# Kernel optimization log

Hardware: AMD Instinct MI355X
Metric: run time of the kernel (lower is better)

## Reference

```python
import jax, jax.numpy as jnp
import numpy as np
import math

D_MODEL = 1024
N_HEAD = 16
D_K = D_MODEL // N_HEAD
NEG_INF = -1e30  # fp32 mask fill value used by the torch module


def _rope(x, b_rotate=None):
    # x: [b, h, n, k], k even. Interleaved (even/odd) RoPE, matching the torch code.
    b, h, n, k = x.shape
    half = k // 2
    inv_freq = 1.0 / (10000.0 ** (jnp.arange(half, dtype=jnp.float32) / half))  # [half]
    ang = jnp.arange(n, dtype=jnp.float32)[:, None] * inv_freq[None, :]          # [n, half]
    sin = jnp.sin(ang)
    cos = jnp.cos(ang)
    x1 = x[..., 0::2]  # [b,h,n,half]
    x2 = x[..., 1::2]
    even = x1 * cos - x2 * sin
    odd = x1 * sin + x2 * cos
    out = jnp.stack([even, odd], axis=-1).reshape(b, h, n, k)  # re-interleave
    if b_rotate is not None:
        out = out * b_rotate  # barope multiplicative term
    return out


def setup_inputs() -> dict:
    key = jax.random.key(0)
    ks = jax.random.split(key, 7)
    B, S = 1, 2048
    query = jax.random.normal(ks[0], (B, S, D_MODEL), dtype=jnp.float32)
    kk = jax.random.normal(ks[1], (B, S, D_MODEL), dtype=jnp.float32)
    value = jax.random.normal(ks[2], (B, S, D_MODEL), dtype=jnp.float32)
    b_emb = jax.random.normal(ks[3], (B, S, D_MODEL), dtype=jnp.float32)
    mask = jax.random.bernoulli(ks[4], 0.9, (B, S))  # bool [B,S]
    linear_layers = 0.02 * jax.random.normal(ks[5], (3, D_MODEL, N_HEAD, D_K), dtype=jnp.float32)
    b_proj = jax.random.normal(ks[6], (D_MODEL, N_HEAD, D_K), dtype=jnp.float32)
    return {"query": query, "key": kk, "value": value, "b_emb": b_emb,
            "mask": mask, "linear_layers": linear_layers, "b_proj": b_proj}


def reference(query, key, value, b_emb, mask, linear_layers, b_proj):
    B, S, _ = query.shape
    # QKV projections: [b,n,d] x [d,h,k] -> [b,h,n,k]
    q = jnp.einsum('bnd,dhk->bhnk', query, linear_layers[0])
    k = jnp.einsum('bnd,dhk->bhnk', key, linear_layers[1])
    v = jnp.einsum('bnd,dhk->bhnk', value, linear_layers[2])
    # barope=True branch: multiplicative rotation modifier from b_emb
    b_rotate = jnp.einsum('bnd,dhk->bhnk', b_emb, b_proj)
    q = _rope(q, b_rotate)
    k = _rope(k, b_rotate)
    scores = jnp.einsum('bhqk,bhmk->bhqm', q, k) / math.sqrt(D_K)  # [b,h,s,s]
    pair_mask = (mask[:, :, None] & mask[:, None, :])[:, None]     # [b,1,s,s]
    scores = jnp.where(pair_mask, scores, NEG_INF)
    p_attn = jax.nn.softmax(scores, axis=-1)  # dropout p=0 -> identity
    x = jnp.einsum('bhqm,bhmk->bhqk', p_attn, v)
    return x.transpose(0, 2, 1, 3).reshape(B, S, N_HEAD * D_K)
```

## Files before the change

kernel.cpp:

```cpp
#include <hip/hip_runtime.h>
#include <hip/hip_bf16.h>
#include <math.h>

#define S_LEN 2048
#define NHEAD 16
#define DMODEL 1024

typedef short bf16x8 __attribute__((ext_vector_type(8)));
typedef float f32x4 __attribute__((ext_vector_type(4)));

static __device__ __forceinline__ unsigned short bfbits(float x) {
    __hip_bfloat16 h = __float2bfloat16(x);
    unsigned short u; __builtin_memcpy(&u, &h, 2); return u;
}
static __device__ __forceinline__ float bf2f(unsigned short u) {
    union { unsigned int i; float f; } v; v.i = ((unsigned int)u) << 16; return v.f;
}
static __device__ __forceinline__ void splitRN(float x, unsigned short& hi, unsigned short& lo) {
    unsigned short h = bfbits(x);
    float r = x - bf2f(h);
    hi = h; lo = bfbits(r);
}
static __device__ __forceinline__ void split4(float4 x, ushort4& h4, ushort4& l4) {
    unsigned short h0,l0,h1,l1,h2,l2,h3,l3;
    splitRN(x.x,h0,l0); splitRN(x.y,h1,l1); splitRN(x.z,h2,l2); splitRN(x.w,h3,l3);
    h4 = make_ushort4(h0,h1,h2,h3); l4 = make_ushort4(l0,l1,l2,l3);
}

__device__ __forceinline__ int mask_at(const void* mp, int enc, int s) {
    if (enc) return ((const unsigned char*)mp)[s] != 0;
    return ((const unsigned int*)mp)[s] != 0u;
}

__global__ void detect_kernel(const void* __restrict__ mask, int* __restrict__ flags) {
    if (threadIdx.x == 0 && blockIdx.x == 0) {
        const unsigned int* m = (const unsigned int*)mask;
        int bytey = 0;
        for (int i = 0; i < 8; ++i) {
            unsigned int u = m[i];
            if (u != 0u && u != 1u && u != 0x3F800000u) bytey = 1;
        }
        flags[0] = bytey;
    }
}

__global__ __launch_bounds__(256)
void presplit_w(const float* __restrict__ ll, const float* __restrict__ bproj,
                unsigned short* __restrict__ Wh, unsigned short* __restrict__ Wl) {
    __shared__ unsigned short Th[64][72], Tl[64][72];
    const int t = threadIdx.x;
    const int bid = blockIdx.x;
    const int stream = bid >> 8;
    const int rem = bid & 255;
    const int h = rem >> 4;
    const int d0 = (rem & 15) << 6;
    const float* src = (stream == 3) ? bproj : (ll + (size_t)stream * 1048576);
#pragma unroll
    for (int rep = 0; rep < 4; ++rep) {
        int fid = rep * 256 + t;
        int dl = fid >> 4, n4 = (fid & 15) * 4;
        float4 w = *(const float4*)&src[(size_t)(d0 + dl) * 1024 + h * 64 + n4];
        unsigned short hh, lo2;
#pragma unroll
        for (int m = 0; m < 4; ++m) { splitRN((&w.x)[m], hh, lo2); Th[n4+m][dl] = hh; Tl[n4+m][dl] = lo2; }
    }
    __syncthreads();
    size_t obase = (size_t)stream * 1048576;
#pragma unroll
    for (int rep = 0; rep < 2; ++rep) {
        int wid = rep * 256 + t;
        int n = wid >> 3, dl8 = (wid & 7) * 8;
        int dtile = n >> 4, cc = n & 15;
        int dglob = d0 + dl8;
        int kc = dglob >> 5;
        int qd = (dglob >> 3) & 3;
        size_t off = obase + (size_t)(h * 4 + dtile) * 16384 + (size_t)kc * 512
                   + (size_t)(qd * 16 + cc) * 8;
        *(uint4*)&Wh[off] = *(uint4*)&Th[n][dl8];
        *(uint4*)&Wl[off] = *(uint4*)&Tl[n][dl8];
    }
}

__global__ __launch_bounds__(256, 4)
void proj_fused7(const float* __restrict__ Xq, const float* __restrict__ Xk,
                 const float* __restrict__ Xv, const float* __restrict__ Xb,
                 const unsigned short* __restrict__ Wh, const unsigned short* __restrict__ Wl,
                 unsigned short* __restrict__ qhi, unsigned short* __restrict__ qlo,
                 unsigned short* __restrict__ khi, unsigned short* __restrict__ klo,
                 unsigned short* __restrict__ vhi) {
    __shared__ unsigned short smem[17920];
    unsigned short (*T0)[72] = (unsigned short(*)[72])(smem + 0);
    unsigned short (*T1)[72] = (unsigned short(*)[72])(smem + 2304);
    unsigned short (*T2)[40] = (unsigned short(*)[40])(smem + 4608);

    const int t = threadIdx.x;
    const int lin = blockIdx.x;
    const int xcd = lin & 7;
    const int inner = lin >> 3;
    const int h = inner >> 3;
    const int sg = inner & 7;
    const int s0 = (xcd * 8 + sg) * 32;
    const int lane = t & 63, dt = t >> 6, quad = lane >> 4, c = lane & 15;

    f32x4 aq[2], ak[2], av[2], ab[2];
#pragma unroll
    for (int i = 0; i < 2; ++i) {
        aq[i] = (f32x4){0.f,0.f,0.f,0.f}; ak[i] = (f32x4){0.f,0.f,0.f,0.f};
        av[i] = (f32x4){0.f,0.f,0.f,0.f}; ab[i] = (f32x4){0.f,0.f,0.f,0.f};
    }

    const int xr = t >> 3, xc = (t & 7) * 4;
    const size_t xg = (size_t)(s0 + xr) * DMODEL + xc;
    const size_t wb = (size_t)(h * 4 + dt) * 16384 + (size_t)lane * 8;

#define XARR(name, b, i) unsigned short (*name)[40] = (unsigned short(*)[40])(smem + (b) * 8960 + (i) * 1280)

    float4 pq, pk, pv, pb;
    pq = *(const float4*)&Xq[xg];
    pk = *(const float4*)&Xk[xg];
    pv = *(const float4*)&Xv[xg];
    pb = *(const float4*)&Xb[xg];
    {
        XARR(XQh,0,0); XARR(XQl,0,1); XARR(XKh,0,2); XARR(XKl,0,3);
        XARR(XVh,0,4); XARR(XBh,0,5); XARR(XBl,0,6);
        ushort4 h4, l4;
        split4(pq, h4, l4); *(ushort4*)&XQh[xr][xc] = h4; *(ushort4*)&XQl[xr][xc] = l4;
        split4(pk, h4, l4); *(ushort4*)&XKh[xr][xc] = h4; *(ushort4*)&XKl[xr][xc] = l4;
        split4(pb, h4, l4); *(ushort4*)&XBh[xr][xc] = h4; *(ushort4*)&XBl[xr][xc] = l4;
        *(ushort4*)&XVh[xr][xc] = make_ushort4(bfbits(pv.x),bfbits(pv.y),bfbits(pv.z),bfbits(pv.w));
    }
    pq = *(const float4*)&Xq[xg + 32];
    pk = *(const float4*)&Xk[xg + 32];
    pv = *(const float4*)&Xv[xg + 32];
    pb = *(const float4*)&Xb[xg + 32];
    __syncthreads();

    for (int kc = 0; kc < 32; ++kc) {
        const int cb = kc & 1, nb = cb ^ 1;
        size_t wo = wb + (size_t)kc * 512;
        bf16x8 aQh = *(const bf16x8*)&Wh[wo];
        bf16x8 aQl = *(const bf16x8*)&Wl[wo];
        bf16x8 aKh = *(const bf16x8*)&Wh[1048576 + wo];
        bf16x8 aKl = *(const bf16x8*)&Wl[1048576 + wo];
        bf16x8 aVh = *(const bf16x8*)&Wh[2097152 + wo];
        bf16x8 aVl = *(const bf16x8*)&Wl[2097152 + wo];
        bf16x8 aBh = *(const bf16x8*)&Wh[3145728 + wo];
        bf16x8 aBl = *(const bf16x8*)&Wl[3145728 + wo];

        if (kc + 1 < 32) {
            XARR(XQh,nb,0); XARR(XQl,nb,1); XARR(XKh,nb,2); XARR(XKl,nb,3);
            XARR(XVh,nb,4); XARR(XBh,nb,5); XARR(XBl,nb,6);
            ushort4 h4, l4;
            split4(pq, h4, l4); *(ushort4*)&XQh[xr][xc] = h4; *(ushort4*)&XQl[xr][xc] = l4;
            split4(pk, h4, l4); *(ushort4*)&XKh[xr][xc] = h4; *(ushort4*)&XKl[xr][xc] = l4;
            split4(pb, h4, l4); *(ushort4*)&XBh[xr][xc] = h4; *(ushort4*)&XBl[xr][xc] = l4;
            *(ushort4*)&XVh[xr][xc] = make_ushort4(bfbits(pv.x),bfbits(pv.y),bfbits(pv.z),bfbits(pv.w));
        }
        if (kc + 2 < 32) {
            size_t g = xg + (size_t)(kc + 2) * 32;
            pq = *(const float4*)&Xq[g];
            pk = *(const float4*)&Xk[g];
            pv = *(const float4*)&Xv[g];
            pb = *(const float4*)&Xb[g];
        }

        {
            XARR(XQh,cb,0); XARR(XQl,cb,1); XARR(XKh,cb,2); XARR(XKl,cb,3);
            XARR(XVh,cb,4); XARR(XBh,cb,5); XARR(XBl,cb,6);
#pragma unroll
            for (int st = 0; st < 2; ++st) {
                bf16x8 b1 = *(bf16x8*)&XQh[st*16+c][quad*8];
                bf16x8 b2 = *(bf16x8*)&XQl[st*16+c][quad*8];
                aq[st] = __builtin_amdgcn_mfma_f32_16x16x32_bf16(aQh, b1, aq[st], 0, 0, 0);
                aq[st] = __builtin_amdgcn_mfma_f32_16x16x32_bf16(aQh, b2, aq[st], 0, 0, 0);
                aq[st] = __builtin_amdgcn_mfma_f32_16x16x32_bf16(aQl, b1, aq[st], 0, 0, 0);
                b1 = *(bf16x8*)&XKh[st*16+c][quad*8];
                b2 = *(bf16x8*)&XKl[st*16+c][quad*8];
                ak[st] = __builtin_amdgcn_mfma_f32_16x16x32_bf16(aKh, b1, ak[st], 0, 0, 0);
                ak[st] = __builtin_amdgcn_mfma_f32_16x16x32_bf16(aKh, b2, ak[st], 0, 0, 0);
                ak[st] = __builtin_amdgcn_mfma_f32_16x16x32_bf16(aKl, b1, ak[st], 0, 0, 0);
                b1 = *(bf16x8*)&XVh[st*16+c][quad*8];
                av[st] = __builtin_amdgcn_mfma_f32_16x16x32_bf16(aVh, b1, av[st], 0, 0, 0);
                av[st] = __builtin_amdgcn_mfma_f32_16x16x32_bf16(aVl, b1, av[st], 0, 0, 0);
                b1 = *(bf16x8*)&XBh[st*16+c][quad*8];
                b2 = *(bf16x8*)&XBl[st*16+c][quad*8];
                ab[st] = __builtin_amdgcn_mfma_f32_16x16x32_bf16(aBh, b1, ab[st], 0, 0, 0);
                ab[st] = __builtin_amdgcn_mfma_f32_16x16x32_bf16(aBh, b2, ab[st], 0, 0, 0);
                ab[st] = __builtin_amdgcn_mfma_f32_16x16x32_bf16(aBl, b1, ab[st], 0, 0, 0);
            }
        }
        __syncthreads();
    }
#undef XARR

    float rq[2][4], rk[2][4];
    {
        int p0 = dt * 8 + 2 * quad;
        double inv0 = pow(10000.0, -(double)p0 / 32.0);
        double inv1 = pow(10000.0, -(double)(p0 + 1) / 32.0);
#pragma unroll
        for (int st = 0; st < 2; ++st) {
            int s = s0 + st * 16 + c;
            double a0 = (double)s * inv0, a1 = (double)s * inv1;
            float sn0 = (float)sin(a0), cs0 = (float)cos(a0);
            float sn1 = (float)sin(a1), cs1 = (float)cos(a1);
            rq[st][0] = (aq[st][0]*cs0 - aq[st][1]*sn0) * ab[st][0] * 0.125f;
            rq[st][1] = (aq[st][0]*sn0 + aq[st][1]*cs0) * ab[st][1] * 0.125f;
            rq[st][2] = (aq[st][2]*cs1 - aq[st][3]*sn1) * ab[st][2] * 0.125f;
            rq[st][3] = (aq[st][2]*sn1 + aq[st][3]*cs1) * ab[st][3] * 0.125f;
            rk[st][0] = (ak[st][0]*cs0 - ak[st][1]*sn0) * ab[st][0];
            rk[st][1] = (ak[st][0]*sn0 + ak[st][1]*cs0) * ab[st][1];
            rk[st][2] = (ak[st][2]*cs1 - ak[st][3]*sn1) * ab[st][2];
            rk[st][3] = (ak[st][2]*sn1 + ak[st][3]*cs1) * ab[st][3];
        }
    }
    __syncthreads();
#pragma unroll
    for (int st = 0; st < 2; ++st) {
        unsigned short h0,l0,h1,l1,h2,l2,h3,l3;
        splitRN(rq[st][0],h0,l0); splitRN(rq[st][1],h1,l1);
        splitRN(rq[st][2],h2,l2); splitRN(rq[st][3],h3,l3);
        *(ushort4*)&T0[st*16+c][dt*16+4*quad] = make_ushort4(h0,h1,h2,h3);
        *(ushort4*)&T1[st*16+c][dt*16+4*quad] = make_ushort4(l0,l1,l2,l3);
#pragma unroll
        for (int reg = 0; reg < 4; ++reg)
            T2[dt * 16 + 4 * quad + reg][st * 16 + c] = bfbits(av[st][reg]);
    }
    __syncthreads();
    {
        int row = t >> 3, d8 = (t & 7) * 8;
        size_t qb = ((size_t)(h * S_LEN + s0 + row)) * 64 + d8;
        *(uint4*)&qhi[qb] = *(uint4*)&T0[row][d8];
        *(uint4*)&qlo[qb] = *(uint4*)&T1[row][d8];
        int d = t >> 2, s8 = (t & 3) * 8;
        size_t vb = ((size_t)(h * 64 + d)) * S_LEN + s0 + s8;
        *(uint4*)&vhi[vb] = *(uint4*)&T2[d][s8];
    }
    __syncthreads();
#pragma unroll
    for (int st = 0; st < 2; ++st) {
        unsigned short h0,l0,h1,l1,h2,l2,h3,l3;
        splitRN(rk[st][0],h0,l0); splitRN(rk[st][1],h1,l1);
        splitRN(rk[st][2],h2,l2); splitRN(rk[st][3],h3,l3);
        *(ushort4*)&T0[st*16+c][dt*16+4*quad] = make_ushort4(h0,h1,h2,h3);
        *(ushort4*)&T1[st*16+c][dt*16+4*quad] = make_ushort4(l0,l1,l2,l3);
    }
    __syncthreads();
    {
        int row = t >> 3, d8 = (t & 7) * 8;
        size_t qb = ((size_t)(h * S_LEN + s0 + row)) * 64 + d8;
        *(uint4*)&khi[qb] = *(uint4*)&T0[row][d8];
        *(uint4*)&klo[qb] = *(uint4*)&T1[row][d8];
    }
}

__global__ __launch_bounds__(256)
void attn_mfma(const unsigned short* __restrict__ qh, const unsigned short* __restrict__ ql,
               const unsigned short* __restrict__ kh, const unsigned short* __restrict__ kl,
               const unsigned short* __restrict__ vh,
               const void* __restrict__ mask, float* __restrict__ out,
               const int* __restrict__ flags) {
    __shared__ unsigned short Kh[2][64][72], Kl[2][64][72];
    __shared__ unsigned short Vt[2][64][72];
    __shared__ unsigned short Sh[64][72], Sl[64][72];
    const int menc = flags[0];
    const int t = threadIdx.x;
    const int lin = blockIdx.x + (blockIdx.y << 5);
    const int h = (lin & 7) * 2 + ((lin >> 3) & 1);
    const int s0 = (lin >> 4) * 64;
    const int lane = t & 63, w = t >> 6, quad = lane >> 4, c = lane & 15;

    bf16x8 qfh[2], qfl[2];
#pragma unroll
    for (int ks = 0; ks < 2; ++ks) {
        size_t base = ((size_t)(h * S_LEN + s0 + 16 * w + c)) * 64 + ks * 32 + quad * 8;
        qfh[ks] = *(const bf16x8*)&qh[base];
        qfl[ks] = *(const bf16x8*)&ql[base];
    }
    int mq[4];
#pragma unroll
    for (int i = 0; i < 4; ++i) mq[i] = mask_at(mask, menc, s0 + 16 * w + quad * 4 + i);

    float m_i[4], l_i[4];
#pragma unroll
    for (int i = 0; i < 4; ++i) { m_i[i] = -INFINITY; l_i[i] = 0.0f; }
    f32x4 o_acc[4];
#pragma unroll
    for (int i = 0; i < 4; ++i) o_acc[i] = (f32x4){0.f,0.f,0.f,0.f};

    uint4 pre[6];
#pragma unroll
    for (int i = 0; i < 2; ++i) {
        int id = i * 256 + t, row = id >> 3, col8 = (id & 7) * 8;
        size_t kb = ((size_t)(h * S_LEN + row)) * 64 + col8;
        size_t vb = ((size_t)(h * 64 + row)) * S_LEN + col8;
        pre[0 + i] = *(const uint4*)&kh[kb];
        pre[2 + i] = *(const uint4*)&kl[kb];
        pre[4 + i] = *(const uint4*)&vh[vb];
    }
#pragma unroll
    for (int i = 0; i < 2; ++i) {
        int id = i * 256 + t, row = id >> 3, col8 = (id & 7) * 8;
        *(uint4*)&Kh[0][row][col8] = pre[0 + i];
        *(uint4*)&Kl[0][row][col8] = pre[2 + i];
        *(uint4*)&Vt[0][row][col8] = pre[4 + i];
    }
    __syncthreads();

    int cur = 0;
    for (int kt = 0; kt < 32; ++kt) {
        if (kt + 1 < 32) {
            const int kb0 = (kt + 1) * 64;
#pragma unroll
            for (int i = 0; i < 2; ++i) {
                int id = i * 256 + t, row = id >> 3, col8 = (id & 7) * 8;
                size_t kb = ((size_t)(h * S_LEN + kb0 + row)) * 64 + col8;
                size_t vb = ((size_t)(h * 64 + row)) * S_LEN + kb0 + col8;
                pre[0 + i] = *(const uint4*)&kh[kb];
                pre[2 + i] = *(const uint4*)&kl[kb];
                pre[4 + i] = *(const uint4*)&vh[vb];
            }
        }
        int mk[4];
#pragma unroll
        for (int nt = 0; nt < 4; ++nt) mk[nt] = mask_at(mask, menc, kt * 64 + 16 * nt + c);

        f32x4 sc[4];
#pragma unroll
        for (int i = 0; i < 4; ++i) sc[i] = (f32x4){0.f,0.f,0.f,0.f};
#pragma unroll
        for (int nt = 0; nt < 4; ++nt)
#pragma unroll
            for (int ks = 0; ks < 2; ++ks) {
                bf16x8 kfh = *(bf16x8*)&Kh[cur][nt * 16 + c][ks * 32 + quad * 8];
                bf16x8 kfl = *(bf16x8*)&Kl[cur][nt * 16 + c][ks * 32 + quad * 8];
                sc[nt] = __builtin_amdgcn_mfma_f32_16x16x32_bf16(qfh[ks], kfh, sc[nt], 0, 0, 0);
                sc[nt] = __builtin_amdgcn_mfma_f32_16x16x32_bf16(qfh[ks], kfl, sc[nt], 0, 0, 0);
                sc[nt] = __builtin_amdgcn_mfma_f32_16x16x32_bf16(qfl[ks], kfh, sc[nt], 0, 0, 0);
            }

        float sm[4][4];
#pragma unroll
        for (int nt = 0; nt < 4; ++nt)
#pragma unroll
            for (int reg = 0; reg < 4; ++reg)
                sm[nt][reg] = (mq[reg] && mk[nt]) ? sc[nt][reg] : -1e30f;

        float rmax[4];
#pragma unroll
        for (int reg = 0; reg < 4; ++reg)
            rmax[reg] = fmaxf(fmaxf(sm[0][reg], sm[1][reg]), fmaxf(sm[2][reg], sm[3][reg]));
#pragma unroll
        for (int off = 1; off <= 8; off <<= 1)
#pragma unroll
            for (int reg = 0; reg < 4; ++reg)
                rmax[reg] = fmaxf(rmax[reg], __shfl_xor(rmax[reg], off, 64));

        float mn[4], alpha[4];
#pragma unroll
        for (int reg = 0; reg < 4; ++reg) {
            mn[reg] = fmaxf(m_i[reg], rmax[reg]);
            alpha[reg] = __expf(m_i[reg] - mn[reg]);
            m_i[reg] = mn[reg];
        }

        float rsum[4] = {0.f, 0.f, 0.f, 0.f};
#pragma unroll
        for (int nt = 0; nt < 4; ++nt)
#pragma unroll
            for (int reg = 0; reg < 4; ++reg) {
                float e = __expf(sm[nt][reg] - mn[reg]);
                rsum[reg] += e;
                unsigned short eh, el;
                splitRN(e, eh, el);
                Sh[16 * w + quad * 4 + reg][16 * nt + c] = eh;
                Sl[16 * w + quad * 4 + reg][16 * nt + c] = el;
            }
#pragma unroll
        for (int off = 1; off <= 8; off <<= 1)
#pragma unroll
            for (int reg = 0; reg < 4; ++reg)
                rsum[reg] += __shfl_xor(rsum[reg], off, 64);
#pragma unroll
        for (int reg = 0; reg < 4; ++reg) l_i[reg] = l_i[reg] * alpha[reg] + rsum[reg];
#pragma unroll
        for (int nt = 0; nt < 4; ++nt)
#pragma unroll
            for (int reg = 0; reg < 4; ++reg) o_acc[nt][reg] *= alpha[reg];

        if (kt + 1 < 32) {
            const int nxt = cur ^ 1;
#pragma unroll
            for (int i = 0; i < 2; ++i) {
                int id = i * 256 + t, row = id >> 3, col8 = (id & 7) * 8;
                *(uint4*)&Kh[nxt][row][col8] = pre[0 + i];
                *(uint4*)&Kl[nxt][row][col8] = pre[2 + i];
                *(uint4*)&Vt[nxt][row][col8] = pre[4 + i];
            }
        }
        __syncthreads();

#pragma unroll
        for (int ks = 0; ks < 2; ++ks) {
            bf16x8 pfh = *(bf16x8*)&Sh[16 * w + c][ks * 32 + quad * 8];
            bf16x8 pfl = *(bf16x8*)&Sl[16 * w + c][ks * 32 + quad * 8];
#pragma unroll
            for (int nt = 0; nt < 4; ++nt) {
                bf16x8 vf = *(bf16x8*)&Vt[cur][nt * 16 + c][ks * 32 + quad * 8];
                o_acc[nt] = __builtin_amdgcn_mfma_f32_16x16x32_bf16(pfh, vf, o_acc[nt], 0, 0, 0);
                o_acc[nt] = __builtin_amdgcn_mfma_f32_16x16x32_bf16(pfl, vf, o_acc[nt], 0, 0, 0);
            }
        }
        __syncthreads();
        cur ^= 1;
    }

#pragma unroll
    for (int reg = 0; reg < 4; ++reg) {
        float inv = 1.0f / l_i[reg];
        int row = s0 + 16 * w + quad * 4 + reg;
#pragma unroll
        for (int nt = 0; nt < 4; ++nt)
            out[(size_t)row * 1024 + h * 64 + nt * 16 + c] = o_acc[nt][reg] * inv;
    }
}

extern "C" void kernel_launch(void* const* d_in, const int* in_sizes, int n_in,
                              void* d_out, int out_size, void* d_ws, size_t ws_size,
                              hipStream_t stream) {
    const float* query = (const float*)d_in[0];
    const float* key   = (const float*)d_in[1];
    const float* value = (const float*)d_in[2];
    const float* b_emb = (const float*)d_in[3];
    const void*  mask  = d_in[4];
    const float* ll    = (const float*)d_in[5];
    const float* bproj = (const float*)d_in[6];
    float* out = (float*)d_out;

    const size_t HSD = (size_t)NHEAD * S_LEN * 64;
    char* ws = (char*)d_ws;
    int* flags = (int*)ws;
    unsigned short* qhi = (unsigned short*)(ws + 4096);
    unsigned short* qlo = qhi + HSD;
    unsigned short* khi = qlo + HSD;
    unsigned short* klo = khi + HSD;
    unsigned short* vhi = klo + HSD;
    unsigned short* Wh  = vhi + HSD;
    unsigned short* Wl  = Wh + 4 * 1048576;

    detect_kernel<<<1, 64, 0, stream>>>(mask, flags);
    presplit_w<<<1024, 256, 0, stream>>>(ll, bproj, Wh, Wl);
    proj_fused7<<<1024, 256, 0, stream>>>(query, key, value, b_emb,
                                          Wh, Wl, qhi, qlo, khi, klo, vhi);
    attn_mfma<<<dim3(32, 16), 256, 0, stream>>>(qhi, qlo, khi, klo, vhi, mask, out, flags);
}
```

Before: 264.6 us.

## Split attention KV range across warp pairs with in-block softmax merge

Each block now covers 32 query rows instead of 64, and its four warps form two groups that each handle half of the key/value sequence. This doubles the grid to 1024 blocks. The two partial softmax states are merged at the end through shared memory. The goal is more parallelism and occupancy on the attention kernel. In exchange, each block loads more K/V per query row, holds more prefetch registers, and pays for a final reduction step.

```diff
diff --git a/kernel.cpp b/kernel.cpp
--- a/kernel.cpp
+++ b/kernel.cpp
@@ -260,26 +260,29 @@
                const unsigned short* __restrict__ vh,
                const void* __restrict__ mask, float* __restrict__ out,
                const int* __restrict__ flags) {
-    __shared__ unsigned short Kh[2][64][72], Kl[2][64][72];
-    __shared__ unsigned short Vt[2][64][72];
-    __shared__ unsigned short Sh[64][72], Sl[64][72];
+    __shared__ unsigned short Kh2[2][64][72], Kl2[2][64][72];
+    __shared__ unsigned short Vt2[2][64][72];
+    __shared__ unsigned short Sh[2][32][72], Sl[2][32][72];
     const int menc = flags[0];
     const int t = threadIdx.x;
-    const int lin = blockIdx.x + (blockIdx.y << 5);
-    const int h = (lin & 7) * 2 + ((lin >> 3) & 1);
-    const int s0 = (lin >> 4) * 64;
+    const int lin = blockIdx.x;
+    const int h = ((lin & 7) << 1) + ((lin >> 3) & 1);
+    const int s0 = (lin >> 4) * 32;
     const int lane = t & 63, w = t >> 6, quad = lane >> 4, c = lane & 15;
+    const int rg = w >> 1;
+    const int qr = (w & 1) * 16;
+    const int kvbase = rg * 1024;
 
     bf16x8 qfh[2], qfl[2];
 #pragma unroll
     for (int ks = 0; ks < 2; ++ks) {
-        size_t base = ((size_t)(h * S_LEN + s0 + 16 * w + c)) * 64 + ks * 32 + quad * 8;
+        size_t base = ((size_t)(h * S_LEN + s0 + qr + c)) * 64 + ks * 32 + quad * 8;
         qfh[ks] = *(const bf16x8*)&qh[base];
         qfl[ks] = *(const bf16x8*)&ql[base];
     }
     int mq[4];
 #pragma unroll
-    for (int i = 0; i < 4; ++i) mq[i] = mask_at(mask, menc, s0 + 16 * w + quad * 4 + i);
+    for (int i = 0; i < 4; ++i) mq[i] = mask_at(mask, menc, s0 + qr + quad * 4 + i);
 
     float m_i[4], l_i[4];
 #pragma unroll
@@ -288,42 +291,51 @@
 #pragma unroll
     for (int i = 0; i < 4; ++i) o_acc[i] = (f32x4){0.f,0.f,0.f,0.f};
 
-    uint4 pre[6];
-#pragma unroll
-    for (int i = 0; i < 2; ++i) {
-        int id = i * 256 + t, row = id >> 3, col8 = (id & 7) * 8;
-        size_t kb = ((size_t)(h * S_LEN + row)) * 64 + col8;
-        size_t vb = ((size_t)(h * 64 + row)) * S_LEN + col8;
-        pre[0 + i] = *(const uint4*)&kh[kb];
-        pre[2 + i] = *(const uint4*)&kl[kb];
-        pre[4 + i] = *(const uint4*)&vh[vb];
-    }
-#pragma unroll
-    for (int i = 0; i < 2; ++i) {
-        int id = i * 256 + t, row = id >> 3, col8 = (id & 7) * 8;
-        *(uint4*)&Kh[0][row][col8] = pre[0 + i];
-        *(uint4*)&Kl[0][row][col8] = pre[2 + i];
-        *(uint4*)&Vt[0][row][col8] = pre[4 + i];
-    }
-    __syncthreads();
-
-    int cur = 0;
-    for (int kt = 0; kt < 32; ++kt) {
-        if (kt + 1 < 32) {
-            const int kb0 = (kt + 1) * 64;
+    uint4 pre[12];
+#pragma unroll
+    for (int r = 0; r < 2; ++r)
+#pragma unroll
+        for (int i = 0; i < 2; ++i) {
+            int id = i * 256 + t, row = id >> 3, col8 = (id & 7) * 8;
+            int kv0 = r * 1024;
+            size_t kb = ((size_t)(h * S_LEN + kv0 + row)) * 64 + col8;
+            size_t vb = ((size_t)(h * 64 + row)) * S_LEN + kv0 + col8;
+            pre[r * 6 + 0 + i] = *(const uint4*)&kh[kb];
+            pre[r * 6 + 2 + i] = *(const uint4*)&kl[kb];
+            pre[r * 6 + 4 + i] = *(const uint4*)&vh[vb];
+        }
+
+    for (int kt = 0; kt < 16; ++kt) {
+        if (kt) __syncthreads();
+#pragma unroll
+        for (int r = 0; r < 2; ++r)
 #pragma unroll
             for (int i = 0; i < 2; ++i) {
                 int id = i * 256 + t, row = id >> 3, col8 = (id & 7) * 8;
-                size_t kb = ((size_t)(h * S_LEN + kb0 + row)) * 64 + col8;
-                size_t vb = ((size_t)(h * 64 + row)) * S_LEN + kb0 + col8;
-                pre[0 + i] = *(const uint4*)&kh[kb];
-                pre[2 + i] = *(const uint4*)&kl[kb];
-                pre[4 + i] = *(const uint4*)&vh[vb];
+                *(uint4*)&Kh2[r][row][col8] = pre[r * 6 + 0 + i];
+                *(uint4*)&Kl2[r][row][col8] = pre[r * 6 + 2 + i];
+                *(uint4*)&Vt2[r][row][col8] = pre[r * 6 + 4 + i];
             }
+        __syncthreads();
+
+        if (kt + 1 < 16) {
+#pragma unroll
+            for (int r = 0; r < 2; ++r)
+#pragma unroll
+                for (int i = 0; i < 2; ++i) {
+                    int id = i * 256 + t, row = id >> 3, col8 = (id & 7) * 8;
+                    int kv0 = r * 1024 + (kt + 1) * 64;
+                    size_t kb = ((size_t)(h * S_LEN + kv0 + row)) * 64 + col8;
+                    size_t vb = ((size_t)(h * 64 + row)) * S_LEN + kv0 + col8;
+                    pre[r * 6 + 0 + i] = *(const uint4*)&kh[kb];
+                    pre[r * 6 + 2 + i] = *(const uint4*)&kl[kb];
+                    pre[r * 6 + 4 + i] = *(const uint4*)&vh[vb];
+                }
         }
         int mk[4];
 #pragma unroll
-        for (int nt = 0; nt < 4; ++nt) mk[nt] = mask_at(mask, menc, kt * 64 + 16 * nt + c);
+        for (int nt = 0; nt < 4; ++nt)
+            mk[nt] = mask_at(mask, menc, kvbase + kt * 64 + 16 * nt + c);
 
         f32x4 sc[4];
 #pragma unroll
@@ -332,8 +344,8 @@
         for (int nt = 0; nt < 4; ++nt)
 #pragma unroll
             for (int ks = 0; ks < 2; ++ks) {
-                bf16x8 kfh = *(bf16x8*)&Kh[cur][nt * 16 + c][ks * 32 + quad * 8];
-                bf16x8 kfl = *(bf16x8*)&Kl[cur][nt * 16 + c][ks * 32 + quad * 8];
+                bf16x8 kfh = *(bf16x8*)&Kh2[rg][nt * 16 + c][ks * 32 + quad * 8];
+                bf16x8 kfl = *(bf16x8*)&Kl2[rg][nt * 16 + c][ks * 32 + quad * 8];
                 sc[nt] = __builtin_amdgcn_mfma_f32_16x16x32_bf16(qfh[ks], kfh, sc[nt], 0, 0, 0);
                 sc[nt] = __builtin_amdgcn_mfma_f32_16x16x32_bf16(qfh[ks], kfl, sc[nt], 0, 0, 0);
                 sc[nt] = __builtin_amdgcn_mfma_f32_16x16x32_bf16(qfl[ks], kfh, sc[nt], 0, 0, 0);
@@ -373,8 +385,8 @@
                 rsum[reg] += e;
                 unsigned short eh, el;
                 splitRN(e, eh, el);
-                Sh[16 * w + quad * 4 + reg][16 * nt + c] = eh;
-                Sl[16 * w + quad * 4 + reg][16 * nt + c] = el;
+                Sh[rg][qr + quad * 4 + reg][16 * nt + c] = eh;
+                Sl[rg][qr + quad * 4 + reg][16 * nt + c] = el;
             }
 #pragma unroll
         for (int off = 1; off <= 8; off <<= 1)
@@ -388,40 +400,48 @@
 #pragma unroll
             for (int reg = 0; reg < 4; ++reg) o_acc[nt][reg] *= alpha[reg];
 
-        if (kt + 1 < 32) {
-            const int nxt = cur ^ 1;
-#pragma unroll
-            for (int i = 0; i < 2; ++i) {
-                int id = i * 256 + t, row = id >> 3, col8 = (id & 7) * 8;
-                *(uint4*)&Kh[nxt][row][col8] = pre[0 + i];
-                *(uint4*)&Kl[nxt][row][col8] = pre[2 + i];
-                *(uint4*)&Vt[nxt][row][col8] = pre[4 + i];
-            }
-        }
-        __syncthreads();
-
 #pragma unroll
         for (int ks = 0; ks < 2; ++ks) {
-            bf16x8 pfh = *(bf16x8*)&Sh[16 * w + c][ks * 32 + quad * 8];
-            bf16x8 pfl = *(bf16x8*)&Sl[16 * w + c][ks * 32 + quad * 8];
+            bf16x8 pfh = *(bf16x8*)&Sh[rg][qr + c][ks * 32 + quad * 8];
+            bf16x8 pfl = *(bf16x8*)&Sl[rg][qr + c][ks * 32 + quad * 8];
 #pragma unroll
             for (int nt = 0; nt < 4; ++nt) {
-                bf16x8 vf = *(bf16x8*)&Vt[cur][nt * 16 + c][ks * 32 + quad * 8];
+                bf16x8 vf = *(bf16x8*)&Vt2[rg][nt * 16 + c][ks * 32 + quad * 8];
                 o_acc[nt] = __builtin_amdgcn_mfma_f32_16x16x32_bf16(pfh, vf, o_acc[nt], 0, 0, 0);
                 o_acc[nt] = __builtin_amdgcn_mfma_f32_16x16x32_bf16(pfl, vf, o_acc[nt], 0, 0, 0);
             }
         }
-        __syncthreads();
-        cur ^= 1;
-    }
-
-#pragma unroll
-    for (int reg = 0; reg < 4; ++reg) {
-        float inv = 1.0f / l_i[reg];
-        int row = s0 + 16 * w + quad * 4 + reg;
-#pragma unroll
-        for (int nt = 0; nt < 4; ++nt)
-            out[(size_t)row * 1024 + h * 64 + nt * 16 + c] = o_acc[nt][reg] * inv;
+    }
+
+    float* Ob = (float*)&Kh2[0][0][0];
+    float* Ml = Ob + 32 * 64;
+    float* Ll = Ml + 32;
+    __syncthreads();
+    if (w >= 2) {
+#pragma unroll
+        for (int reg = 0; reg < 4; ++reg) {
+            int row = qr + quad * 4 + reg;
+#pragma unroll
+            for (int nt = 0; nt < 4; ++nt)
+                Ob[row * 64 + nt * 16 + c] = o_acc[nt][reg];
+            if (c == 0) { Ml[row] = m_i[reg]; Ll[row] = l_i[reg]; }
+        }
+    }
+    __syncthreads();
+    if (w < 2) {
+#pragma unroll
+        for (int reg = 0; reg < 4; ++reg) {
+            int row = qr + quad * 4 + reg;
+            float mb = Ml[row], lb = Ll[row];
+            float m = fmaxf(m_i[reg], mb);
+            float fa = __expf(m_i[reg] - m), fb = __expf(mb - m);
+            float inv = 1.0f / (l_i[reg] * fa + lb * fb);
+            int grow = s0 + row;
+#pragma unroll
+            for (int nt = 0; nt < 4; ++nt)
+                out[(size_t)grow * 1024 + h * 64 + nt * 16 + c] =
+                    (o_acc[nt][reg] * fa + Ob[row * 64 + nt * 16 + c] * fb) * inv;
+        }
     }
 }
 
@@ -452,5 +472,5 @@
     presplit_w<<<1024, 256, 0, stream>>>(ll, bproj, Wh, Wl);
     proj_fused7<<<1024, 256, 0, stream>>>(query, key, value, b_emb,
                                           Wh, Wl, qhi, qlo, khi, klo, vhi);
-    attn_mfma<<<dim3(32, 16), 256, 0, stream>>>(qhi, qlo, khi, klo, vhi, mask, out, flags);
-}
+    attn_mfma<<<1024, 256, 0, stream>>>(qhi, qlo, khi, klo, vhi, mask, out, flags);
+}
```

Result: slower. 428.4 us (+61.9%).
